# Kernel optimization log

Hardware: AMD Instinct MI355X
Metric: run time of the kernel (lower is better)

Reference implementation:

```python
import jax, jax.numpy as jnp
import numpy as np

B, D_IN, UNITS = 4096, 1024, 1024


def setup_inputs() -> dict:
    key = jax.random.key(0)
    ks = jax.random.split(key, 8)
    scale = 1.0 / np.sqrt(D_IN + UNITS)
    return {
        "inputs": jax.random.normal(ks[0], (B, D_IN), jnp.float32),
        "hidden_state": jax.random.normal(ks[1], (B, UNITS), jnp.float32),
        "cell_state": jax.random.normal(ks[2], (B, UNITS), jnp.float32),
        "W_f": jax.random.normal(ks[3], (D_IN + UNITS, UNITS), jnp.float32) * scale,
        "b_f": jnp.ones((UNITS,), jnp.float32),  # forget gate bias initialized to ones
        "W_i": jax.random.normal(ks[4], (D_IN + UNITS, UNITS), jnp.float32) * scale,
        "b_i": jnp.zeros((UNITS,), jnp.float32),
        "W_c": jax.random.normal(ks[5], (D_IN + UNITS, UNITS), jnp.float32) * scale,
        "b_c": jnp.zeros((UNITS,), jnp.float32),
        "W_o": jax.random.normal(ks[6], (D_IN + UNITS, UNITS), jnp.float32) * scale,
        "b_o": jnp.zeros((UNITS,), jnp.float32),
    }


def reference(inputs, hidden_state, cell_state, W_f, b_f, W_i, b_i, W_c, b_c, W_o, b_o):
    # concat (hidden, inputs) along feature axis -> [B, UNITS + D_IN]
    x = jnp.concatenate((hidden_state, inputs), axis=1)
    # fuse the 4 gate projections into one GEMM: [B, 4*UNITS]
    W = jnp.concatenate((W_f, W_i, W_c, W_o), axis=1)
    b = jnp.concatenate((b_f, b_i, b_c, b_o), axis=0)
    gates = x @ W + b
    f, i, c, o = jnp.split(gates, 4, axis=1)
    forget_gate = jax.nn.sigmoid(f)
    input_gate = jax.nn.sigmoid(i)
    state_candidates = jnp.tanh(c)
    output_gate = jax.nn.sigmoid(o)
    new_cell = forget_gate * cell_state + input_gate * state_candidates
    new_hidden = output_gate * jnp.tanh(new_cell)
    return (new_hidden, new_cell)
```

## Files before the change

### kernel.cpp

```cpp
#include <hip/hip_runtime.h>

#define MDIM 4096
#define KDIM 2048
#define UDIM 1024
#define CMOFF (MDIM * UDIM)
#define THREADS 512

typedef __bf16 bfrag __attribute__((ext_vector_type(8)));
typedef float f32x16 __attribute__((ext_vector_type(16)));

#define GLDS(gsrc, ldst)                                                                  \
  __builtin_amdgcn_global_load_lds((const __attribute__((address_space(1))) void*)(gsrc), \
                                   (__attribute__((address_space(3))) void*)(ldst), 16, 0, 0)

__device__ __forceinline__ unsigned short f2bf(float x) {
  unsigned int u = __float_as_uint(x);
  unsigned int r = (u + 0x7fffu + ((u >> 16) & 1u)) >> 16;
  return (unsigned short)r;
}

__device__ __forceinline__ float fast_sigmoid(float x) { return 1.f / (1.f + __expf(-x)); }

__device__ __forceinline__ float fast_tanh(float x) {
  float ax = fabsf(x);
  float e = __expf(-2.f * ax);
  float r = (1.f - e) / (1.f + e);
  return copysignf(r, x);
}


__global__ void pack_x(const float* __restrict__ hidden, const float* __restrict__ inputs,
                       unsigned short* __restrict__ Apk) {
  __shared__ uint4 t4[2048];
  const int P = blockIdx.x;
  const int S = blockIdx.y;
  const int tid = threadIdx.x;
  const size_t m = (size_t)P * 256 + tid;
  const float* src = (S < 16) ? (hidden + m * 1024 + S * 64) : (inputs + m * 1024 + (S - 16) * 64);
  const float4* s4 = (const float4*)src;
#pragma unroll
  for (int j = 0; j < 8; ++j) {
    float4 v0 = s4[2 * j], v1 = s4[2 * j + 1];
    uint4 g;
    g.x = (unsigned)f2bf(v0.x) | ((unsigned)f2bf(v0.y) << 16);
    g.y = (unsigned)f2bf(v0.z) | ((unsigned)f2bf(v0.w) << 16);
    g.z = (unsigned)f2bf(v1.x) | ((unsigned)f2bf(v1.y) << 16);
    g.w = (unsigned)f2bf(v1.z) | ((unsigned)f2bf(v1.w) << 16);
    t4[j * 256 + tid] = g;
  }
  __syncthreads();
  uint4* dst = (uint4*)(Apk + ((size_t)P * 32 + S) * 16384);
#pragma unroll
  for (int c = 0; c < 8; ++c) dst[c * 256 + tid] = t4[c * 256 + tid];
}

__global__ void pack_w(const float* __restrict__ Wf, const float* __restrict__ Wi,
                       const float* __restrict__ Wc, const float* __restrict__ Wo,
                       unsigned short* __restrict__ Bpk) {
  __shared__ unsigned short t1[4][64][64];
  const int bn = blockIdx.x;
  const int S = blockIdx.y;
  const int tid = threadIdx.x;
  const int q = tid >> 6, kk = tid & 63;
  const float* W = (q == 0) ? Wf : (q == 1) ? Wi : (q == 2) ? Wc : Wo;
  const float* src = W + (size_t)(S * 64 + kk) * UDIM + bn * 64;
#pragma unroll
  for (int i = 0; i < 16; ++i) {
    float4 v = ((const float4*)src)[i];
    t1[q][kk][i * 4 + 0] = f2bf(v.x);
    t1[q][kk][i * 4 + 1] = f2bf(v.y);
    t1[q][kk][i * 4 + 2] = f2bf(v.z);
    t1[q][kk][i * 4 + 3] = f2bf(v.w);
  }
  __syncthreads();
  const int qp = (tid >> 5) & 3;
  const int ul = ((tid >> 7) << 5) + (tid & 31);
  uint4* dst = (uint4*)(Bpk + ((size_t)bn * 32 + S) * 16384);
#pragma unroll
  for (int c = 0; c < 8; ++c) {
    const unsigned short* p = &t1[qp][c * 8][ul];
    uint4 g;
    g.x = (unsigned)p[0] | ((unsigned)p[64] << 16);
    g.y = (unsigned)p[128] | ((unsigned)p[192] << 16);
    g.z = (unsigned)p[256] | ((unsigned)p[320] << 16);
    g.w = (unsigned)p[384] | ((unsigned)p[448] << 16);
    dst[c * 256 + tid] = g;
  }
}

__global__ __launch_bounds__(THREADS, 2) void lstm_gemm(
    const unsigned short* __restrict__ Apk, const unsigned short* __restrict__ Bpk,
    const float* __restrict__ bf_, const float* __restrict__ bi_,
    const float* __restrict__ bc_, const float* __restrict__ bo_,
    const float* __restrict__ cell, float* __restrict__ out) {
  extern __shared__ __bf16 lds[];

  const int tid = threadIdx.x;
  const int lane = tid & 63;
  const int wid = tid >> 6;
  const int wr = wid >> 1;
  const int wc = wid & 1;
  const int cl = lane & 31;
  const int hb = lane >> 5;

  const int wg = blockIdx.x;
  const int swz = (wg & 7) * 32 + (wg >> 3);
  const int P = swz >> 4;
  const int m0 = P * 256;
  const int bn = swz & 15;

  const unsigned short* aP = Apk + (size_t)P * 524288 + (size_t)tid * 8;
  const unsigned short* bP = Bpk + (size_t)bn * 524288 + (size_t)tid * 8;

  f32x16 acc[2][4];
#pragma unroll
  for (int mf = 0; mf < 2; ++mf)
#pragma unroll
    for (int nf = 0; nf < 4; ++nf)
#pragma unroll
      for (int j = 0; j < 16; ++j) acc[mf][nf][j] = 0.f;

  const int aBase = hb * 2048 + (wr * 64 + cl) * 8;
  const int bBase = 16384 + hb * 2048 + (wc * 128 + cl) * 8;

#define STAGE(RING)                                                               \
  do {                                                                            \
    _Pragma("unroll") for (int c = 0; c < 4; ++c)                                 \
        GLDS(aP + c * 4096, lds + (RING) * 32768 + c * 4096 + tid * 8);           \
    _Pragma("unroll") for (int c = 0; c < 4; ++c)                                 \
        GLDS(bP + c * 4096, lds + (RING) * 32768 + 16384 + c * 4096 + tid * 8);   \
    aP += 16384;                                                                  \
    bP += 16384;                                                                  \
  } while (0)

#define STEP_BODY(RING, DO_STAGE)                                                     \
  do {                                                                                \
    asm volatile("s_waitcnt vmcnt(0)" ::: "memory");                                  \
    __builtin_amdgcn_s_barrier();                                                     \
    __builtin_amdgcn_sched_barrier(0);                                                \
    if (DO_STAGE) STAGE((RING) ^ 1);                                                  \
    const __bf16* apl = lds + (RING) * 32768 + aBase;                                 \
    const __bf16* bpl = lds + (RING) * 32768 + bBase;                                 \
    _Pragma("unroll") for (int ks = 0; ks < 4; ++ks) {                                \
      bfrag a0 = *(const bfrag*)(apl + ks * 4096);                                    \
      bfrag a1 = *(const bfrag*)(apl + ks * 4096 + 256);                              \
      bfrag b0 = *(const bfrag*)(bpl + ks * 4096);                                    \
      bfrag b1 = *(const bfrag*)(bpl + ks * 4096 + 256);                              \
      bfrag b2 = *(const bfrag*)(bpl + ks * 4096 + 512);                              \
      bfrag b3 = *(const bfrag*)(bpl + ks * 4096 + 768);                              \
      __builtin_amdgcn_s_setprio(1);                                                  \
      acc[0][0] = __builtin_amdgcn_mfma_f32_32x32x16_bf16(a0, b0, acc[0][0], 0, 0, 0);\
      acc[0][1] = __builtin_amdgcn_mfma_f32_32x32x16_bf16(a0, b1, acc[0][1], 0, 0, 0);\
      acc[0][2] = __builtin_amdgcn_mfma_f32_32x32x16_bf16(a0, b2, acc[0][2], 0, 0, 0);\
      acc[0][3] = __builtin_amdgcn_mfma_f32_32x32x16_bf16(a0, b3, acc[0][3], 0, 0, 0);\
      acc[1][0] = __builtin_amdgcn_mfma_f32_32x32x16_bf16(a1, b0, acc[1][0], 0, 0, 0);\
      acc[1][1] = __builtin_amdgcn_mfma_f32_32x32x16_bf16(a1, b1, acc[1][1], 0, 0, 0);\
      acc[1][2] = __builtin_amdgcn_mfma_f32_32x32x16_bf16(a1, b2, acc[1][2], 0, 0, 0);\
      acc[1][3] = __builtin_amdgcn_mfma_f32_32x32x16_bf16(a1, b3, acc[1][3], 0, 0, 0);\
      __builtin_amdgcn_s_setprio(0);                                                  \
    }                                                                                 \
  } while (0)

  STAGE(0);

  for (int it = 0; it < 15; ++it) {
    STEP_BODY(0, 1);
    STEP_BODY(1, 1);
  }
  STEP_BODY(0, 1);
  STEP_BODY(1, 0);

  const int u = bn * 64 + wc * 32 + cl;
  const float fb = bf_[u], ib = bi_[u], cb = bc_[u], ob = bo_[u];
  const int rbase = m0 + wr * 64 + 4 * hb;
#pragma unroll
  for (int mf = 0; mf < 2; ++mf) {
#pragma unroll
    for (int r = 0; r < 16; ++r) {
      const int m = rbase + mf * 32 + (r & 3) + 8 * (r >> 2);
      float pf = acc[mf][0][r] + fb;
      float pi = acc[mf][1][r] + ib;
      float pc = acc[mf][2][r] + cb;
      float po = acc[mf][3][r] + ob;
      float fg = fast_sigmoid(pf);
      float ig = fast_sigmoid(pi);
      float cc = fast_tanh(pc);
      float og = fast_sigmoid(po);
      float cold = cell[(size_t)m * UDIM + u];
      float cnew = fg * cold + ig * cc;
      out[(size_t)m * UDIM + u] = og * fast_tanh(cnew);
      out[CMOFF + (size_t)m * UDIM + u] = cnew;
    }
  }
}

extern "C" void kernel_launch(void* const* d_in, const int* in_sizes, int n_in,
                              void* d_out, int out_size, void* d_ws, size_t ws_size,
                              hipStream_t stream) {
  const float* inputs = (const float*)d_in[0];
  const float* hidden = (const float*)d_in[1];
  const float* cell = (const float*)d_in[2];
  const float* Wf = (const float*)d_in[3];
  const float* bf = (const float*)d_in[4];
  const float* Wi = (const float*)d_in[5];
  const float* bi = (const float*)d_in[6];
  const float* Wc = (const float*)d_in[7];
  const float* bc = (const float*)d_in[8];
  const float* Wo = (const float*)d_in[9];
  const float* bo = (const float*)d_in[10];
  float* out = (float*)d_out;

  unsigned short* Apk = (unsigned short*)d_ws;
  unsigned short* Bpk = Apk + (size_t)MDIM * KDIM;

  pack_x<<<dim3(16, 32), 256, 0, stream>>>(hidden, inputs, Apk);
  pack_w<<<dim3(16, 32), 256, 0, stream>>>(Wf, Wi, Wc, Wo, Bpk);
  lstm_gemm<<<dim3(256), dim3(THREADS), 131072, stream>>>(Apk, Bpk, bf, bi, bc, bo, cell, out);
}
```

Before: 92.34 us.

## Halve GEMM tile height and K-step to launch twice as many smaller workgroups

Each workgroup shrinks from 512 to 256 threads and from 256 to 128 output rows, and the grid grows from 256 to 512 blocks. The K-step per stage is halved, with the staging and LDS ring layout rewritten to match, cutting LDS use per block from 128KB to 48KB. The aim is to fill all CUs (256 blocks underfill an MI355X) and allow more blocks to be resident per CU. In exchange each block does less work per barrier and B tiles are reloaded by twice as many blocks, raising L2 traffic.

```diff
diff --git a/kernel.cpp b/kernel.cpp
--- a/kernel.cpp
+++ b/kernel.cpp
@@ -4,7 +4,7 @@
 #define KDIM 2048
 #define UDIM 1024
 #define CMOFF (MDIM * UDIM)
-#define THREADS 512
+#define THREADS 256
 
 typedef __bf16 bfrag __attribute__((ext_vector_type(8)));
 typedef float f32x16 __attribute__((ext_vector_type(16)));
@@ -104,13 +104,16 @@
   const int hb = lane >> 5;
 
   const int wg = blockIdx.x;
-  const int swz = (wg & 7) * 32 + (wg >> 3);
-  const int P = swz >> 4;
-  const int m0 = P * 256;
+  const int swz = (wg & 7) * 64 + (wg >> 3);
+  const int hp = swz >> 4;
   const int bn = swz & 15;
-
-  const unsigned short* aP = Apk + (size_t)P * 524288 + (size_t)tid * 8;
-  const unsigned short* bP = Bpk + (size_t)bn * 524288 + (size_t)tid * 8;
+  const int P = hp >> 1;
+  const int hpl = hp & 1;
+  const int m0 = hp * 128;
+
+  const unsigned short* aSrc =
+      Apk + (size_t)P * 524288 + (size_t)((tid >> 7) * 2048 + (hpl * 128 + (tid & 127)) * 8);
+  const unsigned short* bSrc = Bpk + (size_t)bn * 524288 + (size_t)tid * 8;
 
   f32x16 acc[2][4];
 #pragma unroll
@@ -120,17 +123,20 @@
 #pragma unroll
       for (int j = 0; j < 16; ++j) acc[mf][nf][j] = 0.f;
 
-  const int aBase = hb * 2048 + (wr * 64 + cl) * 8;
-  const int bBase = 16384 + hb * 2048 + (wc * 128 + cl) * 8;
-
-#define STAGE(RING)                                                               \
-  do {                                                                            \
-    _Pragma("unroll") for (int c = 0; c < 4; ++c)                                 \
-        GLDS(aP + c * 4096, lds + (RING) * 32768 + c * 4096 + tid * 8);           \
-    _Pragma("unroll") for (int c = 0; c < 4; ++c)                                 \
-        GLDS(bP + c * 4096, lds + (RING) * 32768 + 16384 + c * 4096 + tid * 8);   \
-    aP += 16384;                                                                  \
-    bP += 16384;                                                                  \
+  const int aBase = hb * 1024 + (wr * 64 + cl) * 8;
+  const int bBase = 4096 + hb * 2048 + (wc * 128 + cl) * 8;
+
+#define RINGSZ 12288
+#define STAGE(RING)                                                   \
+  do {                                                                \
+    GLDS(aSrc, lds + (RING)*RINGSZ + tid * 8);                        \
+    GLDS(aSrc + 4096, lds + (RING)*RINGSZ + 2048 + tid * 8);          \
+    GLDS(bSrc, lds + (RING)*RINGSZ + 4096 + tid * 8);                 \
+    GLDS(bSrc + 2048, lds + (RING)*RINGSZ + 6144 + tid * 8);          \
+    GLDS(bSrc + 4096, lds + (RING)*RINGSZ + 8192 + tid * 8);          \
+    GLDS(bSrc + 6144, lds + (RING)*RINGSZ + 10240 + tid * 8);         \
+    aSrc += 8192;                                                     \
+    bSrc += 8192;                                                     \
   } while (0)
 
 #define STEP_BODY(RING, DO_STAGE)                                                     \
@@ -139,11 +145,11 @@
     __builtin_amdgcn_s_barrier();                                                     \
     __builtin_amdgcn_sched_barrier(0);                                                \
     if (DO_STAGE) STAGE((RING) ^ 1);                                                  \
-    const __bf16* apl = lds + (RING) * 32768 + aBase;                                 \
-    const __bf16* bpl = lds + (RING) * 32768 + bBase;                                 \
-    _Pragma("unroll") for (int ks = 0; ks < 4; ++ks) {                                \
-      bfrag a0 = *(const bfrag*)(apl + ks * 4096);                                    \
-      bfrag a1 = *(const bfrag*)(apl + ks * 4096 + 256);                              \
+    const __bf16* apl = lds + (RING)*RINGSZ + aBase;                                  \
+    const __bf16* bpl = lds + (RING)*RINGSZ + bBase;                                  \
+    _Pragma("unroll") for (int ks = 0; ks < 2; ++ks) {                                \
+      bfrag a0 = *(const bfrag*)(apl + ks * 2048);                                    \
+      bfrag a1 = *(const bfrag*)(apl + ks * 2048 + 256);                              \
       bfrag b0 = *(const bfrag*)(bpl + ks * 4096);                                    \
       bfrag b1 = *(const bfrag*)(bpl + ks * 4096 + 256);                              \
       bfrag b2 = *(const bfrag*)(bpl + ks * 4096 + 512);                              \
@@ -163,7 +169,7 @@
 
   STAGE(0);
 
-  for (int it = 0; it < 15; ++it) {
+  for (int su = 0; su < 31; ++su) {
     STEP_BODY(0, 1);
     STEP_BODY(1, 1);
   }
@@ -215,5 +221,5 @@
 
   pack_x<<<dim3(16, 32), 256, 0, stream>>>(hidden, inputs, Apk);
   pack_w<<<dim3(16, 32), 256, 0, stream>>>(Wf, Wi, Wc, Wo, Bpk);
-  lstm_gemm<<<dim3(256), dim3(THREADS), 131072, stream>>>(Apk, Bpk, bf, bi, bc, bo, cell, out);
-}
+  lstm_gemm<<<dim3(512), dim3(THREADS), 49152, stream>>>(Apk, Bpk, bf, bi, bc, bo, cell, out);
+}
```

After: 95.03 us. 2.9% more time.
